# Kernel optimization log

Measured on AMD Instinct MI355X. Metric: run time of the kernel, lower is better.

Reference implementation:

```python
import jax, jax.numpy as jnp
import numpy as np

B, L, D, H = 4, 96, 256, 8
HD = D // H
FF = 4 * D
EPS = 1e-5


def _layernorm(x, g, b):
    m = jnp.mean(x, axis=-1, keepdims=True)
    v = jnp.mean((x - m) ** 2, axis=-1, keepdims=True)
    return (x - m) * jax.lax.rsqrt(v + EPS) * g + b


def setup_inputs() -> dict:
    key = jax.random.key(0)
    ks = jax.random.split(key, 12)

    def w(k, shape, fan_in):
        return jax.random.normal(k, shape, jnp.float32) / np.sqrt(fan_in)

    return {
        "table": jax.random.normal(ks[0], (B, L, L, D), jnp.float32),
        "dep_matrix": jax.random.uniform(ks[1], (B, L, L), jnp.float32),
        "Wq": w(ks[2], (D, D), D), "bq": jnp.zeros((D,), jnp.float32),
        "Wk": w(ks[3], (D, D), D), "bk": jnp.zeros((D,), jnp.float32),
        "Wv": w(ks[4], (D, D), D), "bv": jnp.zeros((D,), jnp.float32),
        "Wo": w(ks[5], (D, D), D), "bo": jnp.zeros((D,), jnp.float32),
        "Wdep": w(ks[6], (1, H), 1), "bdep": jnp.zeros((H,), jnp.float32),
        "ln1_g": jnp.ones((D,), jnp.float32), "ln1_b": jnp.zeros((D,), jnp.float32),
        "W1": w(ks[7], (D, FF), D), "b1": jnp.zeros((FF,), jnp.float32),
        "W2": w(ks[8], (FF, D), FF), "b2": jnp.zeros((D,), jnp.float32),
        "ln2_g": jnp.ones((D,), jnp.float32), "ln2_b": jnp.zeros((D,), jnp.float32),
    }


def reference(table, dep_matrix, Wq, bq, Wk, bk, Wv, bv, Wo, bo, Wdep, bdep,
              ln1_g, ln1_b, W1, b1, W2, b2, ln2_g, ln2_b):
    Bx, Lx, _, Dx = table.shape
    Hh = bdep.shape[0]
    hd = Dx // Hh

    def proj(W, b):  # [B,L,L,D] -> [B,H,L,L,hd]
        return (table @ W + b).reshape(Bx, Lx, Lx, Hh, hd).transpose(0, 3, 1, 2, 4)

    q, k, v = proj(Wq, bq), proj(Wk, bk), proj(Wv, bv)

    # attention over last L axis, batched over (B, H, first-L):  [B,H,L,L,L]
    scores = jnp.einsum('bhxqd,bhxkd->bhxqk', q, k) / np.sqrt(hd)

    # learned dependency bias: Linear(1 -> H) on dep_matrix, broadcast over q axis
    dep = dep_matrix[..., None] * Wdep[0] + bdep          # [B,L,L,H]
    dep = dep.transpose(0, 3, 1, 2)[:, :, :, None, :]      # [B,H,L,1,L]

    probs = jax.nn.softmax(scores + dep, axis=-1)          # dropout = identity (eval)

    ctx = jnp.einsum('bhxqk,bhxkd->bhxqd', probs, v)       # [B,H,L,L,hd]
    ctx = ctx.transpose(0, 2, 3, 1, 4).reshape(Bx, Lx, Lx, Dx)

    out = _layernorm(ctx @ Wo + bo + table, ln1_g, ln1_b)
    ff = jax.nn.relu(out @ W1 + b1) @ W2 + b2
    return _layernorm(ff + out, ln2_g, ln2_b)
```

## Files before the change

### kernel.cpp

```cpp
#include <hip/hip_runtime.h>
#include <hip/hip_bf16.h>
#include <math.h>

#define M_ROWS 36864

typedef __bf16 bf16x8 __attribute__((ext_vector_type(8)));
typedef __bf16 bf16x4 __attribute__((ext_vector_type(4)));
typedef float f32x4 __attribute__((ext_vector_type(4)));

__device__ __forceinline__ void gload16(const void* g, void* l) {
  __builtin_amdgcn_global_load_lds((const __attribute__((address_space(1))) void*)g,
                                   (__attribute__((address_space(3))) void*)l, 16, 0, 0);
}

__global__ __launch_bounds__(256) void cvt_bf16_kernel(const float* __restrict__ X,
                                                       __bf16* __restrict__ Y, int n8) {
  int i = blockIdx.x * 256 + threadIdx.x;
  if (i >= n8) return;
  const float4 a = ((const float4*)X)[(size_t)i * 2];
  const float4 b = ((const float4*)X)[(size_t)i * 2 + 1];
  bf16x8 o = {(__bf16)a.x, (__bf16)a.y, (__bf16)a.z, (__bf16)a.w,
              (__bf16)b.x, (__bf16)b.y, (__bf16)b.z, (__bf16)b.w};
  *(bf16x8*)&Y[(size_t)i * 8] = o;
}

__global__ __launch_bounds__(256) void pack_w_kernel(
    const float* __restrict__ Wq, const float* __restrict__ Wk, const float* __restrict__ Wv,
    const float* __restrict__ Wo, const float* __restrict__ W1, const float* __restrict__ W2,
    const float* __restrict__ bq, const float* __restrict__ bk, const float* __restrict__ bv,
    __bf16* __restrict__ Wqkv_t, __bf16* __restrict__ Wo_t,
    __bf16* __restrict__ W1_t, __bf16* __restrict__ W2_t, float* __restrict__ bqkv) {
  int idx = blockIdx.x * 256 + threadIdx.x;
  const int S1 = 768 * 256, S2 = 256 * 256, S3 = 1024 * 256;
  if (idx < S1) {
    int n = idx / 256, k = idx % 256;
    int sel = n >> 8, nn = n & 255;
    const float* W = (sel == 0) ? Wq : (sel == 1) ? Wk : Wv;
    Wqkv_t[idx] = (__bf16)W[k * 256 + nn];
  } else if (idx < S1 + S2) {
    int j = idx - S1; int n = j / 256, k = j % 256;
    Wo_t[j] = (__bf16)Wo[k * 256 + n];
  } else if (idx < S1 + S2 + S3) {
    int j = idx - S1 - S2; int n = j / 256, k = j % 256;
    W1_t[j] = (__bf16)W1[k * 1024 + n];
  } else {
    int j = idx - S1 - S2 - S3; int n = j / 1024, k = j % 1024;
    W2_t[j] = (__bf16)W2[k * 256 + n];
  }
  if (idx < 768) {
    int sel = idx >> 8, jj = idx & 255;
    const float* bsrc = (sel == 0) ? bq : (sel == 1) ? bk : bv;
    bqkv[idx] = bsrc[jj];
  }
}

template <int EPI>
__global__ __launch_bounds__(256, 4) void gemm_small_kernel(
    const __bf16* __restrict__ A, const __bf16* __restrict__ Bt,
    const float* __restrict__ bias, const __bf16* __restrict__ resid,
    __hip_bfloat16* __restrict__ Y, int N, int K) {
  __shared__ __bf16 As[2][64 * 32];
  __shared__ __bf16 Bs[2][128 * 32];
  const int tid = threadIdx.x;
  const int lane = tid & 63, wv = tid >> 6;
  const int wm = wv >> 1, wn = wv & 1;
  const int gx = gridDim.x;
  const int nwg = gx * gridDim.y;
  int lin = blockIdx.y * gx + blockIdx.x;
  lin = (lin & 7) * (nwg >> 3) + (lin >> 3);
  const int n0 = (lin % gx) * 128;
  const int m0 = (lin / gx) * 64;
  const int fr = lane & 15, g = lane >> 4;
  const int rrel = lane >> 2;
  const int gsegA = ((lane & 3) ^ ((lane >> 3) & 3)) * 8;

  f32x4 acc[2][4] = {};
  const int nph = K >> 5;

#define STAGE_S(buf, kb)                                                        \
  {                                                                             \
    gload16(A + (size_t)(m0 + wv * 16 + rrel) * K + (kb) + gsegA,               \
            &As[buf][wv * 512]);                                                \
    gload16(Bt + (size_t)(n0 + wv * 16 + rrel) * K + (kb) + gsegA,              \
            &Bs[buf][wv * 512]);                                                \
    gload16(Bt + (size_t)(n0 + 64 + wv * 16 + rrel) * K + (kb) + gsegA,         \
            &Bs[buf][2048 + wv * 512]);                                         \
  }

  STAGE_S(0, 0)
  __syncthreads();
  int cur = 0;
  for (int p = 0; p < nph; ++p) {
    if (p + 1 < nph) STAGE_S(cur ^ 1, (p + 1) * 32)
    const int cs = (g ^ ((fr >> 1) & 3)) * 8;
    bf16x8 av[2], bv[4];
#pragma unroll
    for (int mi = 0; mi < 2; ++mi)
      av[mi] = *reinterpret_cast<const bf16x8*>(&As[cur][(wm * 32 + mi * 16 + fr) * 32 + cs]);
#pragma unroll
    for (int ni = 0; ni < 4; ++ni)
      bv[ni] = *reinterpret_cast<const bf16x8*>(&Bs[cur][(wn * 64 + ni * 16 + fr) * 32 + cs]);
#pragma unroll
    for (int mi = 0; mi < 2; ++mi)
#pragma unroll
      for (int ni = 0; ni < 4; ++ni)
        acc[mi][ni] = __builtin_amdgcn_mfma_f32_16x16x32_bf16(av[mi], bv[ni], acc[mi][ni], 0, 0, 0);
    __syncthreads();
    cur ^= 1;
  }
#undef STAGE_S

  const int crow = m0 + wm * 32 + g * 4;
  const int ccol = n0 + wn * 64 + fr;
#pragma unroll
  for (int mi = 0; mi < 2; ++mi) {
#pragma unroll
    for (int ni = 0; ni < 4; ++ni) {
      const int col = ccol + ni * 16;
      const float bb = bias[col];
#pragma unroll
      for (int r = 0; r < 4; ++r) {
        const int row = crow + mi * 16 + r;
        float v = acc[mi][ni][r] + bb;
        if (EPI == 1) v = fmaxf(v, 0.f);
        if (EPI == 2) v += (float)resid[(size_t)row * N + col];
        Y[(size_t)row * N + col] = __float2bfloat16(v);
      }
    }
  }
}

template <bool F32OUT>
__global__ __launch_bounds__(256) void ln_bf16_kernel(const __bf16* __restrict__ X,
                                                      const float* __restrict__ gam,
                                                      const float* __restrict__ bet,
                                                      void* __restrict__ Yv) {
  const int row = blockIdx.x * 4 + (threadIdx.x >> 6);
  const int lane = threadIdx.x & 63;
  const size_t base = (size_t)row * 256 + lane * 4;
  bf16x4 x4 = *(const bf16x4*)&X[base];
  float xs[4] = {(float)x4[0], (float)x4[1], (float)x4[2], (float)x4[3]};
  float s = xs[0] + xs[1] + xs[2] + xs[3];
  float q = xs[0] * xs[0] + xs[1] * xs[1] + xs[2] * xs[2] + xs[3] * xs[3];
#pragma unroll
  for (int o = 32; o > 0; o >>= 1) { s += __shfl_xor(s, o); q += __shfl_xor(q, o); }
  const float mean = s * (1.0f / 256.0f);
  const float var = q * (1.0f / 256.0f) - mean * mean;
  const float inv = rsqrtf(var + 1e-5f);
  float4 g4 = *(const float4*)&gam[lane * 4];
  float4 b4 = *(const float4*)&bet[lane * 4];
  float gg[4] = {g4.x, g4.y, g4.z, g4.w};
  float bb[4] = {b4.x, b4.y, b4.z, b4.w};
  if (F32OUT) {
    float4 y4;
    float* yp = &y4.x;
#pragma unroll
    for (int j = 0; j < 4; ++j) yp[j] = (xs[j] - mean) * inv * gg[j] + bb[j];
    *(float4*)&((float*)Yv)[base] = y4;
  } else {
    bf16x4 y4;
#pragma unroll
    for (int j = 0; j < 4; ++j) y4[j] = (__bf16)((xs[j] - mean) * inv * gg[j] + bb[j]);
    *(bf16x4*)&((__bf16*)Yv)[base] = y4;
  }
}

__global__ __launch_bounds__(384) void attn_mfma_kernel(
    const __bf16* __restrict__ qkv, const float* __restrict__ depm,
    const float* __restrict__ Wdep, const float* __restrict__ bdep,
    __hip_bfloat16* __restrict__ ctx) {
  __shared__ __bf16 Qs[96][40];
  __shared__ __bf16 Ks[96][40];
  __shared__ __bf16 Vt[32][104];
  __shared__ __bf16 Ps[6][16][104];
  int lin = blockIdx.x;
  lin = (lin & 7) * 384 + (lin >> 3);
  const int h = lin & 7;
  const int sx = lin >> 3;
  const int x = sx % 96;
  const int b = sx / 96;
  const int tid = threadIdx.x;
  const size_t slab = (size_t)(b * 96 + x) * 96;
  const size_t base = slab * 768 + h * 32;
#pragma unroll
  for (int t = 0; t < 3; ++t) {
    const int idx = tid + t * 384;
    const int r = idx / 12, rem = idx % 12, mat = rem >> 2, seg = rem & 3;
    const int d0 = seg * 8;
    bf16x8 v8 = *(const bf16x8*)&qkv[base + (size_t)r * 768 + mat * 256 + d0];
    if (mat == 0)      *(bf16x8*)&Qs[r][d0] = v8;
    else if (mat == 1) *(bf16x8*)&Ks[r][d0] = v8;
    else {
#pragma unroll
      for (int e = 0; e < 8; ++e) Vt[d0 + e][r] = v8[e];
    }
  }
  __syncthreads();
  const int wave = tid >> 6, lane = tid & 63;
  const int fr = lane & 15, g = lane >> 4;
  const int q0 = wave * 16;
  const float wd = Wdep[h], bd = bdep[h];
  float depb[6];
#pragma unroll
  for (int f = 0; f < 6; ++f) depb[f] = depm[slab + fr + 16 * f] * wd + bd;
  const bf16x8 av = *(const bf16x8*)&Qs[q0 + fr][g * 8];
  f32x4 sacc[6];
#pragma unroll
  for (int f = 0; f < 6; ++f) {
    const bf16x8 bv = *(const bf16x8*)&Ks[f * 16 + fr][g * 8];
    sacc[f] = __builtin_amdgcn_mfma_f32_16x16x32_bf16(av, bv, (f32x4){0.f, 0.f, 0.f, 0.f}, 0, 0, 0);
  }
  const float scale = 0.17677669529663687f;
  float ev[6][4];
  float inv[4];
#pragma unroll
  for (int r = 0; r < 4; ++r) {
    float m = -1e30f;
#pragma unroll
    for (int f = 0; f < 6; ++f) {
      ev[f][r] = sacc[f][r] * scale + depb[f];
      m = fmaxf(m, ev[f][r]);
    }
#pragma unroll
    for (int o = 8; o > 0; o >>= 1) m = fmaxf(m, __shfl_xor(m, o));
    float sum = 0.f;
#pragma unroll
    for (int f = 0; f < 6; ++f) { ev[f][r] = __expf(ev[f][r] - m); sum += ev[f][r]; }
#pragma unroll
    for (int o = 8; o > 0; o >>= 1) sum += __shfl_xor(sum, o);
    inv[r] = 1.0f / sum;
  }
#pragma unroll
  for (int f = 0; f < 6; ++f)
#pragma unroll
    for (int r = 0; r < 4; ++r)
      Ps[wave][g * 4 + r][fr + 16 * f] = (__bf16)ev[f][r];
  asm volatile("s_waitcnt lgkmcnt(0)" ::: "memory");
  f32x4 o0 = {0.f, 0.f, 0.f, 0.f}, o1 = {0.f, 0.f, 0.f, 0.f};
#pragma unroll
  for (int s = 0; s < 3; ++s) {
    const bf16x8 pa  = *(const bf16x8*)&Ps[wave][fr][s * 32 + g * 8];
    const bf16x8 vb0 = *(const bf16x8*)&Vt[fr][s * 32 + g * 8];
    const bf16x8 vb1 = *(const bf16x8*)&Vt[16 + fr][s * 32 + g * 8];
    o0 = __builtin_amdgcn_mfma_f32_16x16x32_bf16(pa, vb0, o0, 0, 0, 0);
    o1 = __builtin_amdgcn_mfma_f32_16x16x32_bf16(pa, vb1, o1, 0, 0, 0);
  }
  const size_t orow = (slab + q0 + g * 4) * 256 + h * 32;
#pragma unroll
  for (int r = 0; r < 4; ++r) {
    ctx[orow + (size_t)r * 256 + fr]      = __float2bfloat16(o0[r] * inv[r]);
    ctx[orow + (size_t)r * 256 + 16 + fr] = __float2bfloat16(o1[r] * inv[r]);
  }
}

extern "C" void kernel_launch(void* const* d_in, const int* in_sizes, int n_in,
                              void* d_out, int out_size, void* d_ws, size_t ws_size,
                              hipStream_t stream) {
  (void)in_sizes; (void)n_in; (void)out_size; (void)ws_size;
  const float* table = (const float*)d_in[0];
  const float* depm  = (const float*)d_in[1];
  const float* Wq = (const float*)d_in[2];   const float* bq = (const float*)d_in[3];
  const float* Wk = (const float*)d_in[4];   const float* bk = (const float*)d_in[5];
  const float* Wv = (const float*)d_in[6];   const float* bv = (const float*)d_in[7];
  const float* Wo = (const float*)d_in[8];   const float* bo = (const float*)d_in[9];
  const float* Wdep = (const float*)d_in[10]; const float* bdep = (const float*)d_in[11];
  const float* g1 = (const float*)d_in[12];  const float* be1 = (const float*)d_in[13];
  const float* W1 = (const float*)d_in[14];  const float* b1 = (const float*)d_in[15];
  const float* W2 = (const float*)d_in[16];  const float* b2 = (const float*)d_in[17];
  const float* g2 = (const float*)d_in[18];  const float* be2 = (const float*)d_in[19];

  char* ws = (char*)d_ws;
  size_t off = 0;
  __bf16* qkvb  = (__bf16*)(ws + off); off += (size_t)M_ROWS * 768 * 2;
  __bf16* ctxb  = (__bf16*)(ws + off); off += (size_t)M_ROWS * 256 * 2;
  __bf16* pre1b = (__bf16*)(ws + off); off += (size_t)M_ROWS * 256 * 2;
  __bf16* outbb = (__bf16*)(ws + off); off += (size_t)M_ROWS * 256 * 2;
  __bf16* hidb  = (__bf16*)(ws + off); off += (size_t)M_ROWS * 1024 * 2;
  __bf16* pre2b = (__bf16*)(ws + off); off += (size_t)M_ROWS * 256 * 2;
  __bf16* tabb  = (__bf16*)(ws + off); off += (size_t)M_ROWS * 256 * 2;
  __bf16* Wqkv_t = (__bf16*)(ws + off); off += 768 * 256 * 2;
  __bf16* Wo_t   = (__bf16*)(ws + off); off += 256 * 256 * 2;
  __bf16* W1_t   = (__bf16*)(ws + off); off += 1024 * 256 * 2;
  __bf16* W2_t   = (__bf16*)(ws + off); off += 256 * 1024 * 2;
  float*  bqkv   = (float*)(ws + off);

  cvt_bf16_kernel<<<4608, 256, 0, stream>>>(table, tabb, M_ROWS * 256 / 8);
  pack_w_kernel<<<3072, 256, 0, stream>>>(Wq, Wk, Wv, Wo, W1, W2, bq, bk, bv,
                                          Wqkv_t, Wo_t, W1_t, W2_t, bqkv);
  gemm_small_kernel<0><<<dim3(6, 576), 256, 0, stream>>>(
      tabb, Wqkv_t, bqkv, nullptr, (__hip_bfloat16*)qkvb, 768, 256);
  attn_mfma_kernel<<<3072, 384, 0, stream>>>(qkvb, depm, Wdep, bdep, (__hip_bfloat16*)ctxb);
  gemm_small_kernel<2><<<dim3(2, 576), 256, 0, stream>>>(
      ctxb, Wo_t, bo, tabb, (__hip_bfloat16*)pre1b, 256, 256);
  ln_bf16_kernel<false><<<9216, 256, 0, stream>>>(pre1b, g1, be1, outbb);
  gemm_small_kernel<1><<<dim3(8, 576), 256, 0, stream>>>(
      outbb, W1_t, b1, nullptr, (__hip_bfloat16*)hidb, 1024, 256);
  gemm_small_kernel<2><<<dim3(2, 576), 256, 0, stream>>>(
      hidb, W2_t, b2, outbb, (__hip_bfloat16*)pre2b, 256, 1024);
  ln_bf16_kernel<true><<<9216, 256, 0, stream>>>(pre2b, g2, be2, (float*)d_out);
}
```

Before: 195.5 us.

## Use single-buffered 64-wide K tiles in small GEMMs with 8-way XOR swizzle

Replaces the double-buffered 32-wide K pipeline of the shared GEMM kernel with single-buffered 64-wide K tiles, so each barrier pair covers twice the MFMA work and the loop runs half as many iterations. The LDS swizzle widens to an 8-segment XOR pattern to match the 64-element rows. It gives up overlap of global loads with compute, since each tile now loads, syncs, then computes, which leaves latency exposed and relies on other resident workgroups to hide it. LDS per block stays the same size.

```diff
diff --git a/kernel.cpp b/kernel.cpp
--- a/kernel.cpp
+++ b/kernel.cpp
@@ -55,12 +55,12 @@
 }
 
 template <int EPI>
-__global__ __launch_bounds__(256, 4) void gemm_small_kernel(
+__global__ __launch_bounds__(256, 4) void gemm_k64_kernel(
     const __bf16* __restrict__ A, const __bf16* __restrict__ Bt,
     const float* __restrict__ bias, const __bf16* __restrict__ resid,
     __hip_bfloat16* __restrict__ Y, int N, int K) {
-  __shared__ __bf16 As[2][64 * 32];
-  __shared__ __bf16 Bs[2][128 * 32];
+  __shared__ __bf16 As[64 * 64];
+  __shared__ __bf16 Bs[128 * 64];
   const int tid = threadIdx.x;
   const int lane = tid & 63, wv = tid >> 6;
   const int wm = wv >> 1, wn = wv & 1;
@@ -71,44 +71,42 @@
   const int n0 = (lin % gx) * 128;
   const int m0 = (lin / gx) * 64;
   const int fr = lane & 15, g = lane >> 4;
-  const int rrel = lane >> 2;
-  const int gsegA = ((lane & 3) ^ ((lane >> 3) & 3)) * 8;
+  const int lrow8 = lane >> 3;
+  const int gseg = ((lane & 7) ^ ((lane >> 3) & 7)) * 8;
 
   f32x4 acc[2][4] = {};
-  const int nph = K >> 5;
-
-#define STAGE_S(buf, kb)                                                        \
-  {                                                                             \
-    gload16(A + (size_t)(m0 + wv * 16 + rrel) * K + (kb) + gsegA,               \
-            &As[buf][wv * 512]);                                                \
-    gload16(Bt + (size_t)(n0 + wv * 16 + rrel) * K + (kb) + gsegA,              \
-            &Bs[buf][wv * 512]);                                                \
-    gload16(Bt + (size_t)(n0 + 64 + wv * 16 + rrel) * K + (kb) + gsegA,         \
-            &Bs[buf][2048 + wv * 512]);                                         \
-  }
-
-  STAGE_S(0, 0)
-  __syncthreads();
-  int cur = 0;
+  const int nph = K >> 6;
+
   for (int p = 0; p < nph; ++p) {
-    if (p + 1 < nph) STAGE_S(cur ^ 1, (p + 1) * 32)
-    const int cs = (g ^ ((fr >> 1) & 3)) * 8;
-    bf16x8 av[2], bv[4];
-#pragma unroll
-    for (int mi = 0; mi < 2; ++mi)
-      av[mi] = *reinterpret_cast<const bf16x8*>(&As[cur][(wm * 32 + mi * 16 + fr) * 32 + cs]);
-#pragma unroll
-    for (int ni = 0; ni < 4; ++ni)
-      bv[ni] = *reinterpret_cast<const bf16x8*>(&Bs[cur][(wn * 64 + ni * 16 + fr) * 32 + cs]);
-#pragma unroll
-    for (int mi = 0; mi < 2; ++mi)
-#pragma unroll
-      for (int ni = 0; ni < 4; ++ni)
-        acc[mi][ni] = __builtin_amdgcn_mfma_f32_16x16x32_bf16(av[mi], bv[ni], acc[mi][ni], 0, 0, 0);
+    const int kb = p * 64;
     __syncthreads();
-    cur ^= 1;
-  }
-#undef STAGE_S
+    gload16(A + (size_t)(m0 + wv * 16 + lrow8) * K + kb + gseg,       &As[wv * 1024]);
+    gload16(A + (size_t)(m0 + wv * 16 + 8 + lrow8) * K + kb + gseg,   &As[wv * 1024 + 512]);
+#pragma unroll
+    for (int j = 0; j < 4; ++j)
+      gload16(Bt + (size_t)(n0 + wv * 32 + j * 8 + lrow8) * K + kb + gseg,
+              &Bs[wv * 2048 + j * 512]);
+    __syncthreads();
+#pragma unroll
+    for (int s = 0; s < 2; ++s) {
+      bf16x8 av[2], bv[4];
+#pragma unroll
+      for (int mi = 0; mi < 2; ++mi) {
+        const int row = wm * 32 + mi * 16 + fr;
+        av[mi] = *reinterpret_cast<const bf16x8*>(&As[row * 64 + (((s * 4 + g) ^ (fr & 7)) * 8)]);
+      }
+#pragma unroll
+      for (int ni = 0; ni < 4; ++ni) {
+        const int row = wn * 64 + ni * 16 + fr;
+        bv[ni] = *reinterpret_cast<const bf16x8*>(&Bs[row * 64 + (((s * 4 + g) ^ (fr & 7)) * 8)]);
+      }
+#pragma unroll
+      for (int mi = 0; mi < 2; ++mi)
+#pragma unroll
+        for (int ni = 0; ni < 4; ++ni)
+          acc[mi][ni] = __builtin_amdgcn_mfma_f32_16x16x32_bf16(av[mi], bv[ni], acc[mi][ni], 0, 0, 0);
+    }
+  }
 
   const int crow = m0 + wm * 32 + g * 4;
   const int ccol = n0 + wn * 64 + fr;
@@ -287,15 +285,15 @@
   cvt_bf16_kernel<<<4608, 256, 0, stream>>>(table, tabb, M_ROWS * 256 / 8);
   pack_w_kernel<<<3072, 256, 0, stream>>>(Wq, Wk, Wv, Wo, W1, W2, bq, bk, bv,
                                           Wqkv_t, Wo_t, W1_t, W2_t, bqkv);
-  gemm_small_kernel<0><<<dim3(6, 576), 256, 0, stream>>>(
+  gemm_k64_kernel<0><<<dim3(6, 576), 256, 0, stream>>>(
       tabb, Wqkv_t, bqkv, nullptr, (__hip_bfloat16*)qkvb, 768, 256);
   attn_mfma_kernel<<<3072, 384, 0, stream>>>(qkvb, depm, Wdep, bdep, (__hip_bfloat16*)ctxb);
-  gemm_small_kernel<2><<<dim3(2, 576), 256, 0, stream>>>(
+  gemm_k64_kernel<2><<<dim3(2, 576), 256, 0, stream>>>(
       ctxb, Wo_t, bo, tabb, (__hip_bfloat16*)pre1b, 256, 256);
   ln_bf16_kernel<false><<<9216, 256, 0, stream>>>(pre1b, g1, be1, outbb);
-  gemm_small_kernel<1><<<dim3(8, 576), 256, 0, stream>>>(
+  gemm_k64_kernel<1><<<dim3(8, 576), 256, 0, stream>>>(
       outbb, W1_t, b1, nullptr, (__hip_bfloat16*)hidb, 1024, 256);
-  gemm_small_kernel<2><<<dim3(2, 576), 256, 0, stream>>>(
+  gemm_k64_kernel<2><<<dim3(2, 576), 256, 0, stream>>>(
       hidb, W2_t, b2, outbb, (__hip_bfloat16*)pre2b, 256, 1024);
   ln_bf16_kernel<true><<<9216, 256, 0, stream>>>(pre2b, g2, be2, (float*)d_out);
 }
```

Result: faster. 182.7 us (-6.6%).
